# Kernel optimization log

Measured on AMD Instinct MI355X. Metric: run time of the kernel, lower is better.

## Reference

```python
import jax, jax.numpy as jnp
import numpy as np

N, E, F, D, H, HID, OUT, G = 25000, 400000, 128, 16, 64, 128, 32, 64

def silu(v):
    return v * jax.nn.sigmoid(v)

def setup_inputs() -> dict:
    key = jax.random.key(0)
    ks = jax.random.split(key, 32)
    inp = {
        'x': jax.random.normal(ks[0], (N, F), jnp.float32),
        'pos': jax.random.normal(ks[1], (N, 3), jnp.float32),
        'edge_attr': jax.random.normal(ks[2], (E, D), jnp.float32),
        'edge_index': jax.random.randint(ks[3], (2, E), 0, N, jnp.int64),
        'batch': jnp.sort(jax.random.randint(ks[4], (N,), 0, G, jnp.int64)),
    }
    def lin(k, fan_in, fan_out):
        return jax.random.normal(k, (fan_in, fan_out), jnp.float32) / np.sqrt(fan_in)
    i = 5
    for l, in_c in enumerate([F, HID]):
        cat = 2 * in_c + D + 1
        inp[f'l{l}_mlp_w'] = lin(ks[i], cat, H); i += 1
        inp[f'l{l}_edge_w'] = lin(ks[i], H, H); i += 1
        inp[f'l{l}_edge_b'] = jnp.zeros((H,), jnp.float32)
        inp[f'l{l}_coord_w'] = lin(ks[i], H, 1); i += 1
        inp[f'l{l}_coord_b'] = jnp.zeros((1,), jnp.float32)
        inp[f'l{l}_node_w1'] = lin(ks[i], in_c + H, H); i += 1
        inp[f'l{l}_node_b1'] = jnp.zeros((H,), jnp.float32)
        inp[f'l{l}_node_w2'] = lin(ks[i], H, HID); i += 1
        inp[f'l{l}_node_b2'] = jnp.zeros((HID,), jnp.float32)
    inp['out_w1'] = lin(ks[i], HID, HID); i += 1
    inp['out_b1'] = jnp.zeros((HID,), jnp.float32)
    inp['out_w2'] = lin(ks[i], HID, OUT); i += 1
    inp['out_b2'] = jnp.zeros((OUT,), jnp.float32)
    return inp

def egnn_layer(x, pos, src, dst, edge_attr, mlp_w, edge_w, edge_b, coord_w, coord_b, nw1, nb1, nw2, nb2):
    # PyG flow source_to_target: i = dst (edge_index[1]), j = src (edge_index[0])
    diff = pos[dst] - pos[src]                    # (E,3)
    radial = jnp.sum(diff * diff, axis=1, keepdims=True)  # (E,1)
    cat = jnp.concatenate([x[dst], x[src], edge_attr, radial], axis=1)
    h = silu(cat @ mlp_w)                         # (E,H)
    e_ij = silu(h @ edge_w + edge_b)              # (E,H)
    coord_update = diff * silu(e_ij @ coord_w + coord_b)  # (E,3)
    e_agg = jax.ops.segment_sum(e_ij, dst, num_segments=N)          # sum reduce
    cu_sum = jax.ops.segment_sum(coord_update, dst, num_segments=N)
    deg = jax.ops.segment_sum(jnp.ones((E, 1), x.dtype), dst, num_segments=N)
    cu_mean = cu_sum / jnp.maximum(deg, 1.0)      # mean reduce, 0 for isolated nodes
    h_node = silu(jnp.concatenate([x, e_agg], axis=1) @ nw1 + nb1) @ nw2 + nb2
    return h_node, pos + cu_mean

def reference(x, pos, edge_attr, edge_index, batch,
              l0_mlp_w, l0_edge_w, l0_edge_b, l0_coord_w, l0_coord_b, l0_node_w1, l0_node_b1, l0_node_w2, l0_node_b2,
              l1_mlp_w, l1_edge_w, l1_edge_b, l1_coord_w, l1_coord_b, l1_node_w1, l1_node_b1, l1_node_w2, l1_node_b2,
              out_w1, out_b1, out_w2, out_b2):
    src, dst = edge_index[0], edge_index[1]
    x, pos = egnn_layer(x, pos, src, dst, edge_attr, l0_mlp_w, l0_edge_w, l0_edge_b, l0_coord_w, l0_coord_b, l0_node_w1, l0_node_b1, l0_node_w2, l0_node_b2)
    x, pos = egnn_layer(x, pos, src, dst, edge_attr, l1_mlp_w, l1_edge_w, l1_edge_b, l1_coord_w, l1_coord_b, l1_node_w1, l1_node_b1, l1_node_w2, l1_node_b2)
    # graph mean pooling over batch assignment
    g_sum = jax.ops.segment_sum(x, batch, num_segments=G)
    g_cnt = jax.ops.segment_sum(jnp.ones((N, 1), x.dtype), batch, num_segments=G)
    g = g_sum / jnp.maximum(g_cnt, 1.0)           # (G, HID)
    g = jax.nn.relu(g)
    return jax.nn.relu(g @ out_w1 + out_b1) @ out_w2 + out_b2  # (G, OUT)
```

## Files before the change

### kernel.cpp

```cpp
#include <hip/hip_runtime.h>
#include <math.h>

#define NN 25000
#define EE 400000
#define FF 128
#define DD 16
#define HH 64
#define HIDC 128
#define OUTC 32
#define GG 64

typedef __attribute__((ext_vector_type(8))) short short8;
typedef __attribute__((ext_vector_type(8))) unsigned short u16x8;
typedef __attribute__((ext_vector_type(4))) float f32x4;

union S8 { short8 v; unsigned short u[8]; };
union U8 { u16x8 v; unsigned short u[8]; };

__device__ __forceinline__ float silu_f(float v) {
    return v / (1.f + __expf(-v));
}

__device__ __forceinline__ unsigned short f2bf_rne(float f) {
  unsigned u = __float_as_uint(f);
  unsigned r = u + 0x7fffu + ((u >> 16) & 1u);
  return (unsigned short)(r >> 16);
}
__device__ __forceinline__ float bfbits2f(unsigned short b) {
  return __uint_as_float(((unsigned)b) << 16);
}

__global__ __launch_bounds__(256) void k_hist(
    const int* __restrict__ ei, int* __restrict__ cnt) {
  const int t = blockIdx.x * 256 + threadIdx.x;
  if (t < EE) atomicAdd(&cnt[ei[EE + t]], 1);
}

__global__ __launch_bounds__(1024) void k_scan(
    const int* __restrict__ cnt, int* __restrict__ row_ptr, int* __restrict__ next) {
  __shared__ int s[1024];
  const int t = threadIdx.x;
  const int base = t * 25;
  int loc[25];
  int sum = 0;
#pragma unroll
  for (int i = 0; i < 25; ++i) {
    const int n = base + i;
    loc[i] = (n < NN) ? cnt[n] : 0;
    sum += loc[i];
  }
  s[t] = sum;
  __syncthreads();
  for (int off = 1; off < 1024; off <<= 1) {
    const int v = (t >= off) ? s[t - off] : 0;
    __syncthreads();
    s[t] += v;
    __syncthreads();
  }
  int run = s[t] - sum;
#pragma unroll
  for (int i = 0; i < 25; ++i) {
    const int n = base + i;
    if (n < NN) {
      row_ptr[n] = run;
      next[n] = run;
      run += loc[i];
    }
  }
  if (t == 0) row_ptr[NN] = EE;
}

__global__ __launch_bounds__(256) void k_scatter(
    const int* __restrict__ ei, const float* __restrict__ eattr, int* __restrict__ next,
    int* __restrict__ sdst, int* __restrict__ ssrc, float* __restrict__ seattr) {
  const int t = blockIdx.x * 256 + threadIdx.x;
  if (t < EE) {
    const int d = ei[EE + t];
    const int slot = atomicAdd(&next[d], 1);
    sdst[slot] = d;
    ssrc[slot] = ei[t];
    const f32x4* s4 = (const f32x4*)&eattr[(size_t)t * DD];
    f32x4* d4 = (f32x4*)&seattr[(size_t)slot * DD];
    d4[0] = s4[0]; d4[1] = s4[1]; d4[2] = s4[2]; d4[3] = s4[3];
  }
}

__global__ __launch_bounds__(256) void k_precompute(
    const float* __restrict__ X, const float* __restrict__ W,
    float* __restrict__ P1, unsigned short* __restrict__ P2h) {
  __shared__ __align__(16) float xT[4][128 * 12];
  const int w = threadIdx.x >> 6, lane = threadIdx.x & 63;
  float* xt = xT[w];
  const int nb = (blockIdx.x * 4 + w) * 8;
#pragma unroll
  for (int e = 0; e < 8; ++e) {
    const int n = nb + e;
    const bool v = n < NN;
    xt[lane * 12 + e]        = v ? X[n * FF + lane] : 0.f;
    xt[(lane + 64) * 12 + e] = v ? X[n * FF + 64 + lane] : 0.f;
  }
  __syncthreads();
  float a1[8], a2[8];
#pragma unroll
  for (int e = 0; e < 8; ++e) { a1[e] = 0.f; a2[e] = 0.f; }
#pragma unroll 4
  for (int k = 0; k < 128; ++k) {
    const float wa = W[k * 64 + lane];
    const float wb = W[(128 + k) * 64 + lane];
    float xk[8];
    *(f32x4*)&xk[0] = *(const f32x4*)&xt[k * 12];
    *(f32x4*)&xk[4] = *(const f32x4*)&xt[k * 12 + 4];
#pragma unroll
    for (int e = 0; e < 8; ++e) {
      a1[e] = fmaf(xk[e], wa, a1[e]);
      a2[e] = fmaf(xk[e], wb, a2[e]);
    }
  }
#pragma unroll
  for (int e = 0; e < 8; ++e) {
    const int n = nb + e;
    if (n < NN) {
      P1[n * 64 + lane]  = a1[e];
      P2h[n * 64 + lane] = f2bf_rne(a2[e]);
    }
  }
}

template <bool COORD>
__global__ __launch_bounds__(256, 4) void k_edge(
    const float* __restrict__ P1, const unsigned short* __restrict__ P2h,
    const float* __restrict__ pos, const float* __restrict__ seattr,
    const int* __restrict__ sdst, const int* __restrict__ ssrc,
    const float* __restrict__ mlp_w,
    const float* __restrict__ edge_w, const float* __restrict__ edge_b,
    const float* __restrict__ coord_w, const float* __restrict__ coord_b,
    float* __restrict__ e_agg, float* __restrict__ cu) {
  __shared__ __align__(16) float s_hs[4][16 * 76];
  __shared__ float s_diff[4][48];
  __shared__ float s_rad[4][16];
  __shared__ float s_red[4][16];
  const int tid = threadIdx.x, w = tid >> 6, lane = tid & 63;
  const int q = lane >> 4, m = lane & 15;

  S8 wB[2][4];
#pragma unroll
  for (int kc = 0; kc < 2; ++kc)
#pragma unroll
    for (int nc = 0; nc < 4; ++nc)
#pragma unroll
      for (int j = 0; j < 8; ++j)
        wB[kc][nc].u[j] = f2bf_rne(edge_w[(kc * 32 + q * 8 + j) * 64 + nc * 16 + m]);
  S8 w3B[4];
#pragma unroll
  for (int nc = 0; nc < 4; ++nc)
#pragma unroll
    for (int j = 0; j < 8; ++j)
      w3B[nc].u[j] = (lane < 32) ? f2bf_rne(mlp_w[256 * 64 + (q * 8 + j) * 64 + nc * 16 + m])
                                 : (unsigned short)0;
  float w4r[4], cwr[4], ebr[4];
#pragma unroll
  for (int nc = 0; nc < 4; ++nc) {
    w4r[nc] = mlp_w[272 * 64 + nc * 16 + m];
    ebr[nc] = edge_b[nc * 16 + m];
    cwr[nc] = COORD ? coord_w[nc * 16 + m] : 0.f;
  }
  const float cb = COORD ? coord_b[0] : 0.f;

  const int wave_id = blockIdx.x * 4 + w;
  const int g0 = wave_id * 6 + (wave_id < 424 ? wave_id : 424);
  const int ng = (wave_id < 424) ? 7 : 6;

  const int pe = (lane < 48) ? (lane / 3) : 0;
  const int pc = lane - (lane / 3) * 3;

  int cur_dst = -1;
  float accum = 0.f;

  for (int g = 0; g < ng; ++g) {
    const int eb = (g0 + g) * 16;
    const int dm = sdst[eb + m];
    const int sm = ssrc[eb + m];
    f32x4 p1a[2], p1b[2];
    U8 p2r[2];
#pragma unroll
    for (int kc = 0; kc < 2; ++kc) {
      const float* pp1 = P1 + (size_t)dm * 64 + kc * 32 + q * 8;
      p1a[kc] = *(const f32x4*)pp1;
      p1b[kc] = *(const f32x4*)(pp1 + 4);
      p2r[kc].v = *(const u16x8*)(P2h + (size_t)sm * 64 + kc * 32 + q * 8);
    }
    if (lane < 48) {
      const int de = __shfl(dm, pe, 64), se = __shfl(sm, pe, 64);
      s_diff[w][lane] = pos[de * 3 + pc] - pos[se * 3 + pc];
    }
    float ea[8] = {0.f, 0.f, 0.f, 0.f, 0.f, 0.f, 0.f, 0.f};
    if (lane < 32) {
      const float* ep = &seattr[(size_t)(eb + m) * DD + q * 8];
      *(f32x4*)&ea[0] = *(const f32x4*)ep;
      *(f32x4*)&ea[4] = *(const f32x4*)(ep + 4);
    }
    S8 eaA;
#pragma unroll
    for (int j = 0; j < 8; ++j) eaA.u[j] = f2bf_rne(ea[j]);
    if (lane < 16) {
      const float d0 = s_diff[w][lane * 3 + 0];
      const float d1 = s_diff[w][lane * 3 + 1];
      const float d2 = s_diff[w][lane * 3 + 2];
      s_rad[w][lane] = fmaf(d0, d0, fmaf(d1, d1, d2 * d2));
    }
    float radr[4];
#pragma unroll
    for (int r = 0; r < 4; ++r) radr[r] = s_rad[w][q * 4 + r];
    f32x4 c3[4];
#pragma unroll
    for (int nc = 0; nc < 4; ++nc) {
      f32x4 z = {0.f, 0.f, 0.f, 0.f};
      c3[nc] = __builtin_amdgcn_mfma_f32_16x16x32_bf16(eaA.v, w3B[nc].v, z, 0, 0, 0);
    }
#pragma unroll
    for (int nc = 0; nc < 4; ++nc)
#pragma unroll
      for (int r = 0; r < 4; ++r)
        s_hs[w][(q * 4 + r) * 76 + nc * 16 + m] = fmaf(radr[r], w4r[nc], c3[nc][r]);
    S8 ahi[2], alo[2];
#pragma unroll
    for (int kc = 0; kc < 2; ++kc) {
      const float* hp = &s_hs[w][m * 76 + kc * 32 + q * 8];
      f32x4 h0 = *(const f32x4*)hp;
      f32x4 h1 = *(const f32x4*)(hp + 4);
      h0 = h0 + p1a[kc];
      h1 = h1 + p1b[kc];
      float hv[8];
      *(f32x4*)&hv[0] = h0;
      *(f32x4*)&hv[4] = h1;
#pragma unroll
      for (int j = 0; j < 8; ++j) {
        const float h = silu_f(hv[j] + bfbits2f(p2r[kc].u[j]));
        const unsigned short hb = (unsigned short)(__float_as_uint(h) >> 16);
        ahi[kc].u[j] = hb;
        alo[kc].u[j] = f2bf_rne(h - bfbits2f(hb));
      }
    }
    f32x4 o[4];
#pragma unroll
    for (int nc = 0; nc < 4; ++nc) {
      f32x4 bi = {ebr[nc], ebr[nc], ebr[nc], ebr[nc]};
      o[nc] = bi;
    }
#pragma unroll
    for (int kc = 0; kc < 2; ++kc)
#pragma unroll
      for (int nc = 0; nc < 4; ++nc) {
        o[nc] = __builtin_amdgcn_mfma_f32_16x16x32_bf16(ahi[kc].v, wB[kc][nc].v, o[nc], 0, 0, 0);
        o[nc] = __builtin_amdgcn_mfma_f32_16x16x32_bf16(alo[kc].v, wB[kc][nc].v, o[nc], 0, 0, 0);
      }
#pragma unroll
    for (int nc = 0; nc < 4; ++nc)
#pragma unroll
      for (int r = 0; r < 4; ++r) o[nc][r] = silu_f(o[nc][r]);
    if (COORD) {
#pragma unroll
      for (int r = 0; r < 4; ++r) {
        float v = o[0][r] * cwr[0] + o[1][r] * cwr[1] + o[2][r] * cwr[2] + o[3][r] * cwr[3];
        v += __shfl_xor(v, 1, 64);
        v += __shfl_xor(v, 2, 64);
        v += __shfl_xor(v, 4, 64);
        v += __shfl_xor(v, 8, 64);
        if (m == 0) s_red[w][q * 4 + r] = v;
      }
    }
#pragma unroll
    for (int nc = 0; nc < 4; ++nc)
#pragma unroll
      for (int r = 0; r < 4; ++r)
        s_hs[w][(q * 4 + r) * 76 + nc * 16 + m] = o[nc][r];
    for (int e = 0; e < 16; ++e) {
      const int dv = __shfl(dm, e, 64);
      const float v = s_hs[w][e * 76 + lane];
      if (dv == cur_dst) {
        accum += v;
      } else {
        if (cur_dst >= 0) atomicAdd(&e_agg[(size_t)cur_dst * 64 + lane], accum);
        cur_dst = dv;
        accum = v;
      }
    }
    if (COORD) {
      if (lane < 48) {
        const float s = silu_f(s_red[w][pe] + cb);
        atomicAdd(&cu[(size_t)__shfl(dm, pe, 64) * 3 + pc], s_diff[w][lane] * s);
      }
    }
  }
  if (cur_dst >= 0) atomicAdd(&e_agg[(size_t)cur_dst * 64 + lane], accum);
}

__global__ __launch_bounds__(256) void k_node_l0(
    const float* __restrict__ x_in, float* __restrict__ e_agg,
    const float* __restrict__ nw1, const float* __restrict__ nb1,
    const float* __restrict__ nw2, const float* __restrict__ nb2,
    const float* __restrict__ pos_in, const float* __restrict__ cu,
    const int* __restrict__ row_ptr,
    float* __restrict__ x_out, float* __restrict__ pos_out,
    const float* __restrict__ Wn, float* __restrict__ P1,
    unsigned short* __restrict__ P2h) {
  __shared__ __align__(16) float xT[4][192 * 12];
  const int w = threadIdx.x >> 6, lane = threadIdx.x & 63;
  float* xt = xT[w];
  const int nb = (blockIdx.x * 4 + w) * 8;
#pragma unroll
  for (int e = 0; e < 8; ++e) {
    const int n = nb + e;
    const bool v = n < NN;
    xt[lane * 12 + e]         = v ? x_in[n * HIDC + lane] : 0.f;
    xt[(64 + lane) * 12 + e]  = v ? x_in[n * HIDC + 64 + lane] : 0.f;
    xt[(128 + lane) * 12 + e] = v ? e_agg[n * 64 + lane] : 0.f;
    if (v) e_agg[n * 64 + lane] = 0.f;
  }
  __syncthreads();
  float a[8];
#pragma unroll
  for (int e = 0; e < 8; ++e) a[e] = nb1[lane];
#pragma unroll 2
  for (int k = 0; k < 192; ++k) {
    const float wv = nw1[k * 64 + lane];
    float xk[8];
    *(f32x4*)&xk[0] = *(const f32x4*)&xt[k * 12];
    *(f32x4*)&xk[4] = *(const f32x4*)&xt[k * 12 + 4];
#pragma unroll
    for (int e = 0; e < 8; ++e) a[e] = fmaf(xk[e], wv, a[e]);
  }
#pragma unroll
  for (int e = 0; e < 8; ++e) a[e] = silu_f(a[e]);
  {
    f32x4 t0 = {a[0], a[1], a[2], a[3]};
    f32x4 t1 = {a[4], a[5], a[6], a[7]};
    *(f32x4*)&xt[lane * 12]     = t0;
    *(f32x4*)&xt[lane * 12 + 4] = t1;
  }
  float olo[8], ohi[8];
#pragma unroll
  for (int e = 0; e < 8; ++e) { olo[e] = nb2[lane]; ohi[e] = nb2[64 + lane]; }
#pragma unroll 2
  for (int k = 0; k < 64; ++k) {
    const float wl = nw2[k * HIDC + lane];
    const float wh = nw2[k * HIDC + 64 + lane];
    float hk[8];
    *(f32x4*)&hk[0] = *(const f32x4*)&xt[k * 12];
    *(f32x4*)&hk[4] = *(const f32x4*)&xt[k * 12 + 4];
#pragma unroll
    for (int e = 0; e < 8; ++e) {
      olo[e] = fmaf(hk[e], wl, olo[e]);
      ohi[e] = fmaf(hk[e], wh, ohi[e]);
    }
  }
#pragma unroll
  for (int e = 0; e < 8; ++e) {
    const int n = nb + e;
    if (n < NN) {
      x_out[n * HIDC + lane]      = olo[e];
      x_out[n * HIDC + 64 + lane] = ohi[e];
    }
  }
#pragma unroll
  for (int e = 0; e < 8; ++e) {
    const int n = nb + e;
    if (n < NN && lane < 3) {
      const float dg = fmaxf((float)(row_ptr[n + 1] - row_ptr[n]), 1.f);
      pos_out[n * 3 + lane] = pos_in[n * 3 + lane] + cu[n * 3 + lane] / dg;
    }
  }
  {
    f32x4 t0 = {olo[0], olo[1], olo[2], olo[3]};
    f32x4 t1 = {olo[4], olo[5], olo[6], olo[7]};
    *(f32x4*)&xt[lane * 12]     = t0;
    *(f32x4*)&xt[lane * 12 + 4] = t1;
    f32x4 t2 = {ohi[0], ohi[1], ohi[2], ohi[3]};
    f32x4 t3 = {ohi[4], ohi[5], ohi[6], ohi[7]};
    *(f32x4*)&xt[(64 + lane) * 12]     = t2;
    *(f32x4*)&xt[(64 + lane) * 12 + 4] = t3;
  }
  float a1[8], a2[8];
#pragma unroll
  for (int e = 0; e < 8; ++e) { a1[e] = 0.f; a2[e] = 0.f; }
#pragma unroll 4
  for (int k = 0; k < 128; ++k) {
    const float wa = Wn[k * 64 + lane];
    const float wb2 = Wn[(128 + k) * 64 + lane];
    float xk[8];
    *(f32x4*)&xk[0] = *(const f32x4*)&xt[k * 12];
    *(f32x4*)&xk[4] = *(const f32x4*)&xt[k * 12 + 4];
#pragma unroll
    for (int e = 0; e < 8; ++e) {
      a1[e] = fmaf(xk[e], wa, a1[e]);
      a2[e] = fmaf(xk[e], wb2, a2[e]);
    }
  }
#pragma unroll
  for (int e = 0; e < 8; ++e) {
    const int n = nb + e;
    if (n < NN) {
      P1[n * 64 + lane]  = a1[e];
      P2h[n * 64 + lane] = f2bf_rne(a2[e]);
    }
  }
}

__global__ __launch_bounds__(256) void k_node_l1(
    const float* __restrict__ x_in, const float* __restrict__ e_agg,
    const float* __restrict__ nw1, const float* __restrict__ nb1,
    const float* __restrict__ nw2, const float* __restrict__ nb2,
    const int* __restrict__ batch,
    float* __restrict__ g_sum, float* __restrict__ g_cnt) {
  __shared__ __align__(16) float xT[4][192 * 12];
  const int w = threadIdx.x >> 6, lane = threadIdx.x & 63;
  float* xt = xT[w];
  const int nb = (blockIdx.x * 4 + w) * 8;
#pragma unroll
  for (int e = 0; e < 8; ++e) {
    const int n = nb + e;
    const bool v = n < NN;
    xt[lane * 12 + e]         = v ? x_in[n * HIDC + lane] : 0.f;
    xt[(64 + lane) * 12 + e]  = v ? x_in[n * HIDC + 64 + lane] : 0.f;
    xt[(128 + lane) * 12 + e] = v ? e_agg[n * 64 + lane] : 0.f;
  }
  __syncthreads();
  float a[8];
#pragma unroll
  for (int e = 0; e < 8; ++e) a[e] = nb1[lane];
#pragma unroll 2
  for (int k = 0; k < 192; ++k) {
    const float wv = nw1[k * 64 + lane];
    float xk[8];
    *(f32x4*)&xk[0] = *(const f32x4*)&xt[k * 12];
    *(f32x4*)&xk[4] = *(const f32x4*)&xt[k * 12 + 4];
#pragma unroll
    for (int e = 0; e < 8; ++e) a[e] = fmaf(xk[e], wv, a[e]);
  }
#pragma unroll
  for (int e = 0; e < 8; ++e) a[e] = silu_f(a[e]);
  {
    f32x4 t0 = {a[0], a[1], a[2], a[3]};
    f32x4 t1 = {a[4], a[5], a[6], a[7]};
    *(f32x4*)&xt[lane * 12]     = t0;
    *(f32x4*)&xt[lane * 12 + 4] = t1;
  }
  float olo[8], ohi[8];
#pragma unroll
  for (int e = 0; e < 8; ++e) { olo[e] = nb2[lane]; ohi[e] = nb2[64 + lane]; }
#pragma unroll 2
  for (int k = 0; k < 64; ++k) {
    const float wl = nw2[k * HIDC + lane];
    const float wh = nw2[k * HIDC + 64 + lane];
    float hk[8];
    *(f32x4*)&hk[0] = *(const f32x4*)&xt[k * 12];
    *(f32x4*)&hk[4] = *(const f32x4*)&xt[k * 12 + 4];
#pragma unroll
    for (int e = 0; e < 8; ++e) {
      olo[e] = fmaf(hk[e], wl, olo[e]);
      ohi[e] = fmaf(hk[e], wh, ohi[e]);
    }
  }
  int curb = -1;
  float accL = 0.f, accH = 0.f, c = 0.f;
#pragma unroll
  for (int e = 0; e < 8; ++e) {
    const int n = nb + e;
    if (n < NN) {
      const int bg = batch[n];
      if (bg != curb) {
        if (curb >= 0) {
          atomicAdd(&g_sum[curb * HIDC + lane], accL);
          atomicAdd(&g_sum[curb * HIDC + 64 + lane], accH);
          if (lane == 0) atomicAdd(&g_cnt[curb], c);
        }
        curb = bg; accL = olo[e]; accH = ohi[e]; c = 1.f;
      } else {
        accL += olo[e]; accH += ohi[e]; c += 1.f;
      }
    }
  }
  if (curb >= 0) {
    atomicAdd(&g_sum[curb * HIDC + lane], accL);
    atomicAdd(&g_sum[curb * HIDC + 64 + lane], accH);
    if (lane == 0) atomicAdd(&g_cnt[curb], c);
  }
}

__global__ __launch_bounds__(128) void k_final(
    const float* __restrict__ g_sum, const float* __restrict__ g_cnt,
    const float* __restrict__ w1, const float* __restrict__ b1,
    const float* __restrict__ w2, const float* __restrict__ b2,
    float* __restrict__ out) {
  __shared__ float sg[128];
  __shared__ float sh[128];
  const int g = blockIdx.x, j = threadIdx.x;
  const float c = fmaxf(g_cnt[g], 1.f);
  sg[j] = fmaxf(g_sum[g * HIDC + j] / c, 0.f);
  __syncthreads();
  float a = b1[j];
  for (int k = 0; k < 128; ++k) a += sg[k] * w1[k * 128 + j];
  sh[j] = fmaxf(a, 0.f);
  __syncthreads();
  if (j < OUTC) {
    float o = b2[j];
    for (int k = 0; k < 128; ++k) o += sh[k] * w2[k * OUTC + j];
    out[g * OUTC + j] = o;
  }
}

extern "C" void kernel_launch(void* const* d_in, const int* in_sizes, int n_in,
                              void* d_out, int out_size, void* d_ws, size_t ws_size,
                              hipStream_t stream) {
  const float* x     = (const float*)d_in[0];
  const float* pos   = (const float*)d_in[1];
  const float* eattr = (const float*)d_in[2];
  const int*   ei    = (const int*)d_in[3];
  const int*   batch = (const int*)d_in[4];
  const float* mlp_w[2]   = {(const float*)d_in[5],  (const float*)d_in[14]};
  const float* edge_w[2]  = {(const float*)d_in[6],  (const float*)d_in[15]};
  const float* edge_b[2]  = {(const float*)d_in[7],  (const float*)d_in[16]};
  const float* coord_w[2] = {(const float*)d_in[8],  (const float*)d_in[17]};
  const float* coord_b[2] = {(const float*)d_in[9],  (const float*)d_in[18]};
  const float* nw1[2]     = {(const float*)d_in[10], (const float*)d_in[19]};
  const float* nb1[2]     = {(const float*)d_in[11], (const float*)d_in[20]};
  const float* nw2[2]     = {(const float*)d_in[12], (const float*)d_in[21]};
  const float* nb2[2]     = {(const float*)d_in[13], (const float*)d_in[22]};
  const float* ow1 = (const float*)d_in[23];
  const float* ob1 = (const float*)d_in[24];
  const float* ow2 = (const float*)d_in[25];
  const float* ob2 = (const float*)d_in[26];
  float* out = (float*)d_out;

  char* p = (char*)d_ws;
  auto alloc = [&](size_t bytes) {
    void* r = (void*)p;
    p += (bytes + 255) & ~(size_t)255;
    return r;
  };
  float* P1            = (float*)alloc((size_t)NN * 64 * 4);
  unsigned short* P2h  = (unsigned short*)alloc((size_t)NN * 64 * 2);
  float* e_agg         = (float*)alloc((size_t)NN * 64 * 4);
  float* cu            = (float*)alloc((size_t)NN * 3 * 4);
  float* x1            = (float*)alloc((size_t)NN * HIDC * 4);
  float* pos1          = (float*)alloc((size_t)NN * 3 * 4);
  float* g_sum         = (float*)alloc((size_t)GG * HIDC * 4);
  float* g_cnt         = (float*)alloc((size_t)GG * 4);
  int* cnt             = (int*)alloc((size_t)NN * 4);
  int* row_ptr         = (int*)alloc((size_t)(NN + 1) * 4);
  int* nxt             = (int*)alloc((size_t)NN * 4);
  int* sdst            = (int*)alloc((size_t)EE * 4);
  int* ssrc            = (int*)alloc((size_t)EE * 4);
  float* seattr        = (float*)alloc((size_t)EE * DD * 4);

  const int nodeBlocks = (NN + 31) / 32;
  const int edgeBlocks = 1024;

  (void)hipMemsetAsync(e_agg, 0, (size_t)NN * 64 * 4, stream);
  (void)hipMemsetAsync(cu,    0, (size_t)NN * 3 * 4, stream);
  (void)hipMemsetAsync(g_sum, 0, (size_t)GG * HIDC * 4, stream);
  (void)hipMemsetAsync(g_cnt, 0, (size_t)GG * 4, stream);
  (void)hipMemsetAsync(cnt,   0, (size_t)NN * 4, stream);

  k_hist<<<(EE + 255) / 256, 256, 0, stream>>>(ei, cnt);
  k_scan<<<1, 1024, 0, stream>>>(cnt, row_ptr, nxt);
  k_scatter<<<(EE + 255) / 256, 256, 0, stream>>>(ei, eattr, nxt, sdst, ssrc, seattr);

  k_precompute<<<nodeBlocks, 256, 0, stream>>>(x, mlp_w[0], P1, P2h);
  k_edge<true><<<edgeBlocks, 256, 0, stream>>>(P1, P2h, pos, seattr, sdst, ssrc,
      mlp_w[0], edge_w[0], edge_b[0], coord_w[0], coord_b[0], e_agg, cu);
  k_node_l0<<<nodeBlocks, 256, 0, stream>>>(x, e_agg, nw1[0], nb1[0],
      nw2[0], nb2[0], pos, cu, row_ptr, x1, pos1, mlp_w[1], P1, P2h);

  k_edge<false><<<edgeBlocks, 256, 0, stream>>>(P1, P2h, pos1, seattr, sdst, ssrc,
      mlp_w[1], edge_w[1], edge_b[1], coord_w[1], coord_b[1], e_agg, cu);
  k_node_l1<<<nodeBlocks, 256, 0, stream>>>(x1, e_agg, nw1[1], nb1[1],
      nw2[1], nb2[1], batch, g_sum, g_cnt);

  k_final<<<GG, 128, 0, stream>>>(g_sum, g_cnt, ow1, ob1, ow2, ob2, out);
}
```

Baseline: 515.6 us.

## Fuse scatter with precompute and defer edge-attr permutation into first edge kernel

The edge-scatter kernel is merged into the node precompute kernel as extra blocks, so the two run in one launch. The scatter now records only the original edge id, and the first-layer edge kernel gathers edge_attr by that id and writes the sorted copy for layer 1 to reuse. The five separate memsets become one contiguous memset by reordering workspace buffers. This removes a launch, a memset chain and a separate edge-attr copy pass, at the cost of an extra index load and an indirect gather in the layer-0 edge kernel.

```diff
diff --git a/kernel.cpp b/kernel.cpp
--- a/kernel.cpp
+++ b/kernel.cpp
@@ -9,6 +9,8 @@
 #define HIDC 128
 #define OUTC 32
 #define GG 64
+#define NODEBLK 782
+#define SCATBLK 1563
 
 typedef __attribute__((ext_vector_type(8))) short short8;
 typedef __attribute__((ext_vector_type(8))) unsigned short u16x8;
@@ -70,25 +72,23 @@
   if (t == 0) row_ptr[NN] = EE;
 }
 
-__global__ __launch_bounds__(256) void k_scatter(
-    const int* __restrict__ ei, const float* __restrict__ eattr, int* __restrict__ next,
-    int* __restrict__ sdst, int* __restrict__ ssrc, float* __restrict__ seattr) {
-  const int t = blockIdx.x * 256 + threadIdx.x;
-  if (t < EE) {
-    const int d = ei[EE + t];
-    const int slot = atomicAdd(&next[d], 1);
-    sdst[slot] = d;
-    ssrc[slot] = ei[t];
-    const f32x4* s4 = (const f32x4*)&eattr[(size_t)t * DD];
-    f32x4* d4 = (f32x4*)&seattr[(size_t)slot * DD];
-    d4[0] = s4[0]; d4[1] = s4[1]; d4[2] = s4[2]; d4[3] = s4[3];
-  }
-}
-
-__global__ __launch_bounds__(256) void k_precompute(
+__global__ __launch_bounds__(256) void k_sp(
+    const int* __restrict__ ei, int* __restrict__ next,
+    int* __restrict__ sdst, int* __restrict__ ssrc, int* __restrict__ seid,
     const float* __restrict__ X, const float* __restrict__ W,
     float* __restrict__ P1, unsigned short* __restrict__ P2h) {
   __shared__ __align__(16) float xT[4][128 * 12];
+  if (blockIdx.x >= NODEBLK) {
+    const int t = (blockIdx.x - NODEBLK) * 256 + threadIdx.x;
+    if (t < EE) {
+      const int d = ei[EE + t];
+      const int slot = atomicAdd(&next[d], 1);
+      sdst[slot] = d;
+      ssrc[slot] = ei[t];
+      seid[slot] = t;
+    }
+    return;
+  }
   const int w = threadIdx.x >> 6, lane = threadIdx.x & 63;
   float* xt = xT[w];
   const int nb = (blockIdx.x * 4 + w) * 8;
@@ -126,10 +126,11 @@
   }
 }
 
-template <bool COORD>
+template <bool COORD, bool GATHER>
 __global__ __launch_bounds__(256, 4) void k_edge(
     const float* __restrict__ P1, const unsigned short* __restrict__ P2h,
-    const float* __restrict__ pos, const float* __restrict__ seattr,
+    const float* __restrict__ pos, const float* __restrict__ eattr,
+    float* __restrict__ seattr, const int* __restrict__ seid,
     const int* __restrict__ sdst, const int* __restrict__ ssrc,
     const float* __restrict__ mlp_w,
     const float* __restrict__ edge_w, const float* __restrict__ edge_b,
@@ -193,15 +194,28 @@
       const int de = __shfl(dm, pe, 64), se = __shfl(sm, pe, 64);
       s_diff[w][lane] = pos[de * 3 + pc] - pos[se * 3 + pc];
     }
-    float ea[8] = {0.f, 0.f, 0.f, 0.f, 0.f, 0.f, 0.f, 0.f};
+    f32x4 ea0 = {0.f, 0.f, 0.f, 0.f}, ea1 = {0.f, 0.f, 0.f, 0.f};
     if (lane < 32) {
-      const float* ep = &seattr[(size_t)(eb + m) * DD + q * 8];
-      *(f32x4*)&ea[0] = *(const f32x4*)ep;
-      *(f32x4*)&ea[4] = *(const f32x4*)(ep + 4);
+      if (GATHER) {
+        const int eid = seid[eb + m];
+        const float* ep = &eattr[(size_t)eid * DD + q * 8];
+        ea0 = *(const f32x4*)ep;
+        ea1 = *(const f32x4*)(ep + 4);
+        float* sp = &seattr[(size_t)(eb + m) * DD + q * 8];
+        *(f32x4*)sp = ea0;
+        *(f32x4*)(sp + 4) = ea1;
+      } else {
+        const float* ep = &seattr[(size_t)(eb + m) * DD + q * 8];
+        ea0 = *(const f32x4*)ep;
+        ea1 = *(const f32x4*)(ep + 4);
+      }
     }
     S8 eaA;
 #pragma unroll
-    for (int j = 0; j < 8; ++j) eaA.u[j] = f2bf_rne(ea[j]);
+    for (int j = 0; j < 4; ++j) {
+      eaA.u[j]     = f2bf_rne(ea0[j]);
+      eaA.u[4 + j] = f2bf_rne(ea1[j]);
+    }
     if (lane < 16) {
       const float d0 = s_diff[w][lane * 3 + 0];
       const float d1 = s_diff[w][lane * 3 + 1];
@@ -540,41 +554,41 @@
   };
   float* P1            = (float*)alloc((size_t)NN * 64 * 4);
   unsigned short* P2h  = (unsigned short*)alloc((size_t)NN * 64 * 2);
+  char* zero_base      = p;
   float* e_agg         = (float*)alloc((size_t)NN * 64 * 4);
   float* cu            = (float*)alloc((size_t)NN * 3 * 4);
-  float* x1            = (float*)alloc((size_t)NN * HIDC * 4);
-  float* pos1          = (float*)alloc((size_t)NN * 3 * 4);
   float* g_sum         = (float*)alloc((size_t)GG * HIDC * 4);
   float* g_cnt         = (float*)alloc((size_t)GG * 4);
   int* cnt             = (int*)alloc((size_t)NN * 4);
+  const size_t zero_sz = (size_t)(p - zero_base);
   int* row_ptr         = (int*)alloc((size_t)(NN + 1) * 4);
   int* nxt             = (int*)alloc((size_t)NN * 4);
   int* sdst            = (int*)alloc((size_t)EE * 4);
   int* ssrc            = (int*)alloc((size_t)EE * 4);
+  int* seid            = (int*)alloc((size_t)EE * 4);
   float* seattr        = (float*)alloc((size_t)EE * DD * 4);
-
-  const int nodeBlocks = (NN + 31) / 32;
+  float* x1            = (float*)alloc((size_t)NN * HIDC * 4);
+  float* pos1          = (float*)alloc((size_t)NN * 3 * 4);
+
   const int edgeBlocks = 1024;
 
-  (void)hipMemsetAsync(e_agg, 0, (size_t)NN * 64 * 4, stream);
-  (void)hipMemsetAsync(cu,    0, (size_t)NN * 3 * 4, stream);
-  (void)hipMemsetAsync(g_sum, 0, (size_t)GG * HIDC * 4, stream);
-  (void)hipMemsetAsync(g_cnt, 0, (size_t)GG * 4, stream);
-  (void)hipMemsetAsync(cnt,   0, (size_t)NN * 4, stream);
-
-  k_hist<<<(EE + 255) / 256, 256, 0, stream>>>(ei, cnt);
+  (void)hipMemsetAsync(zero_base, 0, zero_sz, stream);
+
+  k_hist<<<SCATBLK, 256, 0, stream>>>(ei, cnt);
   k_scan<<<1, 1024, 0, stream>>>(cnt, row_ptr, nxt);
-  k_scatter<<<(EE + 255) / 256, 256, 0, stream>>>(ei, eattr, nxt, sdst, ssrc, seattr);
-
-  k_precompute<<<nodeBlocks, 256, 0, stream>>>(x, mlp_w[0], P1, P2h);
-  k_edge<true><<<edgeBlocks, 256, 0, stream>>>(P1, P2h, pos, seattr, sdst, ssrc,
-      mlp_w[0], edge_w[0], edge_b[0], coord_w[0], coord_b[0], e_agg, cu);
-  k_node_l0<<<nodeBlocks, 256, 0, stream>>>(x, e_agg, nw1[0], nb1[0],
+  k_sp<<<NODEBLK + SCATBLK, 256, 0, stream>>>(ei, nxt, sdst, ssrc, seid,
+      x, mlp_w[0], P1, P2h);
+
+  k_edge<true, true><<<edgeBlocks, 256, 0, stream>>>(P1, P2h, pos, eattr,
+      seattr, seid, sdst, ssrc, mlp_w[0], edge_w[0], edge_b[0],
+      coord_w[0], coord_b[0], e_agg, cu);
+  k_node_l0<<<NODEBLK, 256, 0, stream>>>(x, e_agg, nw1[0], nb1[0],
       nw2[0], nb2[0], pos, cu, row_ptr, x1, pos1, mlp_w[1], P1, P2h);
 
-  k_edge<false><<<edgeBlocks, 256, 0, stream>>>(P1, P2h, pos1, seattr, sdst, ssrc,
-      mlp_w[1], edge_w[1], edge_b[1], coord_w[1], coord_b[1], e_agg, cu);
-  k_node_l1<<<nodeBlocks, 256, 0, stream>>>(x1, e_agg, nw1[1], nb1[1],
+  k_edge<false, false><<<edgeBlocks, 256, 0, stream>>>(P1, P2h, pos1, eattr,
+      seattr, seid, sdst, ssrc, mlp_w[1], edge_w[1], edge_b[1],
+      coord_w[1], coord_b[1], e_agg, cu);
+  k_node_l1<<<NODEBLK, 256, 0, stream>>>(x1, e_agg, nw1[1], nb1[1],
       nw2[1], nb2[1], batch, g_sum, g_cnt);
 
   k_final<<<GG, 128, 0, stream>>>(g_sum, g_cnt, ow1, ob1, ow2, ob2, out);
```

Result: no change. 507.9 us (-1.5%).
